# Optimization experiments

Measured on AMD Instinct MI355X. Metric: run time of the kernel, lower is better.

## Reference

```python
import jax, jax.numpy as jnp
import numpy as np


def setup_inputs() -> dict:
    key = jax.random.key(0)
    ks = jax.random.split(key, 8)
    B, L, E, D, A = 128, 196, 2048, 1024, 1024
    s_e = 1.0 / np.sqrt(E)
    s_d = 1.0 / np.sqrt(D)
    return {
        "encoder_outputs": jax.random.normal(ks[0], (B, L, E), jnp.float32),
        "decoder_hidden": jax.random.normal(ks[1], (B, D), jnp.float32),
        "Wq": jax.random.normal(ks[2], (A, E), jnp.float32) * s_e,
        "bq": jax.random.normal(ks[3], (A,), jnp.float32) * s_e,
        "Wv": jax.random.normal(ks[4], (A, E), jnp.float32) * s_e,
        "bv": jax.random.normal(ks[5], (A,), jnp.float32) * s_e,
        "Wd": jax.random.normal(ks[6], (A, D), jnp.float32) * s_d,
        "bd": jax.random.normal(ks[7], (A,), jnp.float32) * s_d,
    }


def reference(encoder_outputs, decoder_hidden, Wq, bq, Wv, bv, Wd, bd):
    # get_encoder_features: project encoder outputs to queries/values [B, L, A]
    enc_q = jnp.einsum('ble,ae->bla', encoder_outputs, Wq) + bq
    enc_v = jnp.einsum('ble,ae->bla', encoder_outputs, Wv) + bv
    # forward: project decoder hidden [B, A]
    dec_q = decoder_hidden @ Wd.T + bd
    # attn_energy = bmm(enc_q, dec_q) -> [B, L]; tanh then softmax over L
    energy = jnp.tanh(jnp.einsum('bla,ba->bl', enc_q, dec_q))
    weights = jax.nn.softmax(energy, axis=1)
    # context = bmm(weights, enc_v) -> [B, A]
    context = jnp.einsum('bl,bla->ba', weights, enc_v)
    return context
```

## Files before the change

### kernel.cpp

```cpp
#include <hip/hip_runtime.h>
#include <cstdint>
#include <cstddef>


template <bool BNC>
__global__ __launch_bounds__(256) void gemm_part(
    const float* __restrict__ A, const float* __restrict__ Bm,
    float* __restrict__ part, int M, int N, int K, int kPerZ) {
  __shared__ float As[32][132];
  __shared__ float Bs[32][68];
  const int t = threadIdx.x;
  const int tx = t & 7, ty = t >> 3;
  const int n0 = blockIdx.x * 64;
  const int m0 = blockIdx.y * 128;
  const int z  = blockIdx.z;
  const int k0 = z * kPerZ;

  float acc[4][8];
#pragma unroll
  for (int i = 0; i < 4; ++i)
#pragma unroll
    for (int j = 0; j < 8; ++j) acc[i][j] = 0.f;

  for (int kb = k0; kb < k0 + kPerZ; kb += 32) {
    __syncthreads();
    {
      int m = t >> 1, kq = (t & 1) * 16;
      const float* src = A + (size_t)(m0 + m) * K + (kb + kq);
      float4 v0 = *(const float4*)(src + 0);
      float4 v1 = *(const float4*)(src + 4);
      float4 v2 = *(const float4*)(src + 8);
      float4 v3 = *(const float4*)(src + 12);
      As[kq + 0][m] = v0.x; As[kq + 1][m] = v0.y; As[kq + 2][m] = v0.z; As[kq + 3][m] = v0.w;
      As[kq + 4][m] = v1.x; As[kq + 5][m] = v1.y; As[kq + 6][m] = v1.z; As[kq + 7][m] = v1.w;
      As[kq + 8][m] = v2.x; As[kq + 9][m] = v2.y; As[kq + 10][m] = v2.z; As[kq + 11][m] = v2.w;
      As[kq + 12][m] = v3.x; As[kq + 13][m] = v3.y; As[kq + 14][m] = v3.z; As[kq + 15][m] = v3.w;
    }
    if (BNC) {
      int kk = t >> 3, nq = (t & 7) * 8;
      const float* src = Bm + (size_t)(kb + kk) * N + (n0 + nq);
      float4 v0 = *(const float4*)(src + 0);
      float4 v1 = *(const float4*)(src + 4);
      *(float4*)&Bs[kk][nq + 0] = v0;
      *(float4*)&Bs[kk][nq + 4] = v1;
    } else {
      int n = t >> 2, kq = (t & 3) * 8;
      const float* src = Bm + (size_t)(n0 + n) * K + (kb + kq);
      float4 v0 = *(const float4*)(src + 0);
      float4 v1 = *(const float4*)(src + 4);
      Bs[kq + 0][n] = v0.x; Bs[kq + 1][n] = v0.y; Bs[kq + 2][n] = v0.z; Bs[kq + 3][n] = v0.w;
      Bs[kq + 4][n] = v1.x; Bs[kq + 5][n] = v1.y; Bs[kq + 6][n] = v1.z; Bs[kq + 7][n] = v1.w;
    }
    __syncthreads();
#pragma unroll 4
    for (int kk = 0; kk < 32; ++kk) {
      float av[4], bv[8];
      *(float4*)&av[0] = *(const float4*)&As[kk][ty * 4];
      *(float4*)&bv[0] = *(const float4*)&Bs[kk][tx * 8 + 0];
      *(float4*)&bv[4] = *(const float4*)&Bs[kk][tx * 8 + 4];
#pragma unroll
      for (int i = 0; i < 4; ++i)
#pragma unroll
        for (int j = 0; j < 8; ++j) acc[i][j] = fmaf(av[i], bv[j], acc[i][j]);
    }
  }
  float* dst = part + (size_t)z * M * N;
#pragma unroll
  for (int i = 0; i < 4; ++i) {
    int m = m0 + ty * 4 + i;
    float4 lo = make_float4(acc[i][0], acc[i][1], acc[i][2], acc[i][3]);
    float4 hi = make_float4(acc[i][4], acc[i][5], acc[i][6], acc[i][7]);
    *(float4*)&dst[(size_t)m * N + n0 + tx * 8 + 0] = lo;
    *(float4*)&dst[(size_t)m * N + n0 + tx * 8 + 4] = hi;
  }
}

__global__ __launch_bounds__(256) void reduce_part(
    const float* __restrict__ part, const float* __restrict__ bias,
    float* __restrict__ out, int MN, int N, int Z) {
  int i = blockIdx.x * 256 + threadIdx.x;
  if (i * 4 >= MN) return;
  float4 a = make_float4(0.f, 0.f, 0.f, 0.f);
  for (int z = 0; z < Z; ++z) {
    float4 v = *(const float4*)&part[(size_t)z * MN + i * 4];
    a.x += v.x; a.y += v.y; a.z += v.z; a.w += v.w;
  }
  if (bias) {
    int n = (i * 4) % N;
    float4 bb = *(const float4*)&bias[n];
    a.x += bb.x; a.y += bb.y; a.z += bb.z; a.w += bb.w;
  }
  *(float4*)&out[(size_t)i * 4] = a;
}

__global__ __launch_bounds__(256) void attn_pass(
    const float* __restrict__ x,
    const float* __restrict__ u,
    const float* __restrict__ dec_q,
    const float* __restrict__ bq,
    float* __restrict__ Yp,
    float* __restrict__ ss) {
  const int L = 196, E = 2048, A = 1024, RPB = 49;
  __shared__ float yS[4][2048];
  __shared__ float red[4];
  __shared__ float sred[4];
  const int t = threadIdx.x;
  const int lane = t & 63, w = t >> 6;
  const int b = blockIdx.x >> 2, q = blockIdx.x & 3;
  const int l0 = q * RPB;

  {
    const float* dq = dec_q + (size_t)b * A;
    float cp = 0.f;
#pragma unroll
    for (int j = 0; j < 4; ++j) cp = fmaf(bq[t + j * 256], dq[t + j * 256], cp);
    for (int off = 32; off; off >>= 1) cp += __shfl_xor(cp, off);
    if (lane == 0) red[w] = cp;
  }
  __syncthreads();
  const float cB = red[0] + red[1] + red[2] + red[3];

  float4 ur[8];
  const float* ub = u + (size_t)b * E;
#pragma unroll
  for (int i = 0; i < 8; ++i) ur[i] = *(const float4*)(ub + lane * 4 + i * 256);

  float4 y[8];
#pragma unroll
  for (int i = 0; i < 8; ++i) y[i] = make_float4(0.f, 0.f, 0.f, 0.f);
  float s = 0.f;

  for (int l = l0 + w; l < l0 + RPB; l += 4) {
    const float* xr = x + ((size_t)b * L + l) * E;
    float4 xv[8];
#pragma unroll
    for (int i = 0; i < 8; ++i) xv[i] = *(const float4*)(xr + lane * 4 + i * 256);
    float d = 0.f;
#pragma unroll
    for (int i = 0; i < 8; ++i) {
      d = fmaf(xv[i].x, ur[i].x, d);
      d = fmaf(xv[i].y, ur[i].y, d);
      d = fmaf(xv[i].z, ur[i].z, d);
      d = fmaf(xv[i].w, ur[i].w, d);
    }
    for (int off = 32; off; off >>= 1) d += __shfl_xor(d, off);
    float wj = __expf(tanhf(d + cB));
    s += wj;
#pragma unroll
    for (int i = 0; i < 8; ++i) {
      y[i].x = fmaf(wj, xv[i].x, y[i].x);
      y[i].y = fmaf(wj, xv[i].y, y[i].y);
      y[i].z = fmaf(wj, xv[i].z, y[i].z);
      y[i].w = fmaf(wj, xv[i].w, y[i].w);
    }
  }

#pragma unroll
  for (int i = 0; i < 8; ++i) *(float4*)&yS[w][lane * 4 + i * 256] = y[i];
  if (lane == 0) sred[w] = s;
  __syncthreads();

#pragma unroll
  for (int h = 0; h < 2; ++h) {
    int pos = t * 4 + h * 1024;
    float4 a0 = *(const float4*)&yS[0][pos];
    float4 a1 = *(const float4*)&yS[1][pos];
    float4 a2 = *(const float4*)&yS[2][pos];
    float4 a3 = *(const float4*)&yS[3][pos];
    float4 a = make_float4(a0.x + a1.x + a2.x + a3.x, a0.y + a1.y + a2.y + a3.y,
                           a0.z + a1.z + a2.z + a3.z, a0.w + a1.w + a2.w + a3.w);
    *(float4*)&Yp[(size_t)blockIdx.x * E + pos] = a;
  }
  if (t == 0) ss[blockIdx.x] = sred[0] + sred[1] + sred[2] + sred[3];
}

__global__ __launch_bounds__(256) void merge_y(
    const float* __restrict__ Yp, const float* __restrict__ ss,
    float* __restrict__ y) {
  const int E = 2048;
  int b = blockIdx.x, t = threadIdx.x;
  float S = ss[b * 4 + 0] + ss[b * 4 + 1] + ss[b * 4 + 2] + ss[b * 4 + 3];
  float inv = 1.f / S;
#pragma unroll
  for (int h = 0; h < 2; ++h) {
    int pos = t * 4 + h * 1024;
    float4 a = make_float4(0.f, 0.f, 0.f, 0.f);
#pragma unroll
    for (int qq = 0; qq < 4; ++qq) {
      float4 v = *(const float4*)&Yp[(size_t)(b * 4 + qq) * E + pos];
      a.x += v.x; a.y += v.y; a.z += v.z; a.w += v.w;
    }
    a.x *= inv; a.y *= inv; a.z *= inv; a.w *= inv;
    *(float4*)&y[(size_t)b * E + pos] = a;
  }
}

extern "C" void kernel_launch(void* const* d_in, const int* in_sizes, int n_in,
                              void* d_out, int out_size, void* d_ws, size_t ws_size,
                              hipStream_t stream) {
  const float* x  = (const float*)d_in[0];
  const float* dh = (const float*)d_in[1];
  const float* Wq = (const float*)d_in[2];
  const float* bq = (const float*)d_in[3];
  const float* Wv = (const float*)d_in[4];
  const float* bv = (const float*)d_in[5];
  const float* Wd = (const float*)d_in[6];
  const float* bd = (const float*)d_in[7];
  float* out = (float*)d_out;
  float* ws = (float*)d_ws;

  float* dec_q = ws;
  float* u     = ws + 131072;
  float* y     = ws + 393216;
  float* Yp    = ws + 655360;
  float* ssb   = ws + 1703936;
  float* part  = ws + 1705984;

  gemm_part<false><<<dim3(16, 1, 32), 256, 0, stream>>>(dh, Wd, part, 128, 1024, 1024, 32);
  reduce_part<<<dim3(128), 256, 0, stream>>>(part, bd, dec_q, 131072, 1024, 32);
  gemm_part<true><<<dim3(32, 1, 16), 256, 0, stream>>>(dec_q, Wq, part, 128, 2048, 1024, 64);
  reduce_part<<<dim3(256), 256, 0, stream>>>(part, nullptr, u, 262144, 2048, 16);
  attn_pass<<<dim3(512), 256, 0, stream>>>(x, u, dec_q, bq, Yp, ssb);
  merge_y<<<dim3(128), 256, 0, stream>>>(Yp, ssb, y);
  gemm_part<false><<<dim3(16, 1, 32), 256, 0, stream>>>(y, Wv, part, 128, 1024, 2048, 64);
  reduce_part<<<dim3(128), 256, 0, stream>>>(part, bv, out, 131072, 1024, 32);
}
```

Baseline: 368.8 us.

## Fuse all stages into one cooperative persistent kernel with grid syncs

Replaces the eight separate launches with a single cooperative kernel of 512 blocks that runs each stage and separates them with grid-wide syncs, falling back to the old multi-launch path if the cooperative launch fails. The attention stage now writes per-wave partial sums straight to global memory instead of reducing them through shared memory, and the merge stage sums 16 partials per batch row. This targets launch overhead and inter-kernel gaps between the small GEMM and reduce stages. In exchange it adds the cost of grid barriers, requires all 512 blocks to be co-resident, and increases the partial-sum traffic in the merge.

```diff
diff --git a/kernel.cpp b/kernel.cpp
--- a/kernel.cpp
+++ b/kernel.cpp
@@ -1,21 +1,20 @@
 #include <hip/hip_runtime.h>
+#include <hip/hip_cooperative_groups.h>
 #include <cstdint>
 #include <cstddef>
 
+namespace cg = cooperative_groups;
+
+
+struct SmGemm { float As[32][132]; float Bs[32][68]; };
 
 template <bool BNC>
-__global__ __launch_bounds__(256) void gemm_part(
+__device__ __forceinline__ void gemm_body(
     const float* __restrict__ A, const float* __restrict__ Bm,
-    float* __restrict__ part, int M, int N, int K, int kPerZ) {
-  __shared__ float As[32][132];
-  __shared__ float Bs[32][68];
-  const int t = threadIdx.x;
+    float* __restrict__ part, int N, int K, int kPerZ, int n0, int z,
+    SmGemm* sm, int t) {
   const int tx = t & 7, ty = t >> 3;
-  const int n0 = blockIdx.x * 64;
-  const int m0 = blockIdx.y * 128;
-  const int z  = blockIdx.z;
   const int k0 = z * kPerZ;
-
   float acc[4][8];
 #pragma unroll
   for (int i = 0; i < 4; ++i)
@@ -26,48 +25,48 @@
     __syncthreads();
     {
       int m = t >> 1, kq = (t & 1) * 16;
-      const float* src = A + (size_t)(m0 + m) * K + (kb + kq);
+      const float* src = A + (size_t)m * K + (kb + kq);
       float4 v0 = *(const float4*)(src + 0);
       float4 v1 = *(const float4*)(src + 4);
       float4 v2 = *(const float4*)(src + 8);
       float4 v3 = *(const float4*)(src + 12);
-      As[kq + 0][m] = v0.x; As[kq + 1][m] = v0.y; As[kq + 2][m] = v0.z; As[kq + 3][m] = v0.w;
-      As[kq + 4][m] = v1.x; As[kq + 5][m] = v1.y; As[kq + 6][m] = v1.z; As[kq + 7][m] = v1.w;
-      As[kq + 8][m] = v2.x; As[kq + 9][m] = v2.y; As[kq + 10][m] = v2.z; As[kq + 11][m] = v2.w;
-      As[kq + 12][m] = v3.x; As[kq + 13][m] = v3.y; As[kq + 14][m] = v3.z; As[kq + 15][m] = v3.w;
+      sm->As[kq + 0][m] = v0.x; sm->As[kq + 1][m] = v0.y; sm->As[kq + 2][m] = v0.z; sm->As[kq + 3][m] = v0.w;
+      sm->As[kq + 4][m] = v1.x; sm->As[kq + 5][m] = v1.y; sm->As[kq + 6][m] = v1.z; sm->As[kq + 7][m] = v1.w;
+      sm->As[kq + 8][m] = v2.x; sm->As[kq + 9][m] = v2.y; sm->As[kq + 10][m] = v2.z; sm->As[kq + 11][m] = v2.w;
+      sm->As[kq + 12][m] = v3.x; sm->As[kq + 13][m] = v3.y; sm->As[kq + 14][m] = v3.z; sm->As[kq + 15][m] = v3.w;
     }
     if (BNC) {
       int kk = t >> 3, nq = (t & 7) * 8;
       const float* src = Bm + (size_t)(kb + kk) * N + (n0 + nq);
       float4 v0 = *(const float4*)(src + 0);
       float4 v1 = *(const float4*)(src + 4);
-      *(float4*)&Bs[kk][nq + 0] = v0;
-      *(float4*)&Bs[kk][nq + 4] = v1;
+      *(float4*)&sm->Bs[kk][nq + 0] = v0;
+      *(float4*)&sm->Bs[kk][nq + 4] = v1;
     } else {
       int n = t >> 2, kq = (t & 3) * 8;
       const float* src = Bm + (size_t)(n0 + n) * K + (kb + kq);
       float4 v0 = *(const float4*)(src + 0);
       float4 v1 = *(const float4*)(src + 4);
-      Bs[kq + 0][n] = v0.x; Bs[kq + 1][n] = v0.y; Bs[kq + 2][n] = v0.z; Bs[kq + 3][n] = v0.w;
-      Bs[kq + 4][n] = v1.x; Bs[kq + 5][n] = v1.y; Bs[kq + 6][n] = v1.z; Bs[kq + 7][n] = v1.w;
+      sm->Bs[kq + 0][n] = v0.x; sm->Bs[kq + 1][n] = v0.y; sm->Bs[kq + 2][n] = v0.z; sm->Bs[kq + 3][n] = v0.w;
+      sm->Bs[kq + 4][n] = v1.x; sm->Bs[kq + 5][n] = v1.y; sm->Bs[kq + 6][n] = v1.z; sm->Bs[kq + 7][n] = v1.w;
     }
     __syncthreads();
 #pragma unroll 4
     for (int kk = 0; kk < 32; ++kk) {
       float av[4], bv[8];
-      *(float4*)&av[0] = *(const float4*)&As[kk][ty * 4];
-      *(float4*)&bv[0] = *(const float4*)&Bs[kk][tx * 8 + 0];
-      *(float4*)&bv[4] = *(const float4*)&Bs[kk][tx * 8 + 4];
+      *(float4*)&av[0] = *(const float4*)&sm->As[kk][ty * 4];
+      *(float4*)&bv[0] = *(const float4*)&sm->Bs[kk][tx * 8 + 0];
+      *(float4*)&bv[4] = *(const float4*)&sm->Bs[kk][tx * 8 + 4];
 #pragma unroll
       for (int i = 0; i < 4; ++i)
 #pragma unroll
         for (int j = 0; j < 8; ++j) acc[i][j] = fmaf(av[i], bv[j], acc[i][j]);
     }
   }
-  float* dst = part + (size_t)z * M * N;
+  float* dst = part + (size_t)z * 128 * N;
 #pragma unroll
   for (int i = 0; i < 4; ++i) {
-    int m = m0 + ty * 4 + i;
+    int m = ty * 4 + i;
     float4 lo = make_float4(acc[i][0], acc[i][1], acc[i][2], acc[i][3]);
     float4 hi = make_float4(acc[i][4], acc[i][5], acc[i][6], acc[i][7]);
     *(float4*)&dst[(size_t)m * N + n0 + tx * 8 + 0] = lo;
@@ -75,59 +74,47 @@
   }
 }
 
-__global__ __launch_bounds__(256) void reduce_part(
+__device__ __forceinline__ void reduce_body(
     const float* __restrict__ part, const float* __restrict__ bias,
-    float* __restrict__ out, int MN, int N, int Z) {
-  int i = blockIdx.x * 256 + threadIdx.x;
-  if (i * 4 >= MN) return;
-  float4 a = make_float4(0.f, 0.f, 0.f, 0.f);
-  for (int z = 0; z < Z; ++z) {
-    float4 v = *(const float4*)&part[(size_t)z * MN + i * 4];
-    a.x += v.x; a.y += v.y; a.z += v.z; a.w += v.w;
-  }
-  if (bias) {
-    int n = (i * 4) % N;
-    float4 bb = *(const float4*)&bias[n];
-    a.x += bb.x; a.y += bb.y; a.z += bb.z; a.w += bb.w;
-  }
-  *(float4*)&out[(size_t)i * 4] = a;
-}
-
-__global__ __launch_bounds__(256) void attn_pass(
-    const float* __restrict__ x,
-    const float* __restrict__ u,
-    const float* __restrict__ dec_q,
-    const float* __restrict__ bq,
-    float* __restrict__ Yp,
-    float* __restrict__ ss) {
+    float* __restrict__ outp, int MN, int N, int Z, int gtid) {
+  if (gtid * 4 < MN) {
+    float4 a = make_float4(0.f, 0.f, 0.f, 0.f);
+    for (int z = 0; z < Z; ++z) {
+      float4 v = *(const float4*)&part[(size_t)z * MN + gtid * 4];
+      a.x += v.x; a.y += v.y; a.z += v.z; a.w += v.w;
+    }
+    if (bias) {
+      int n = (gtid * 4) % N;
+      float4 bb = *(const float4*)&bias[n];
+      a.x += bb.x; a.y += bb.y; a.z += bb.z; a.w += bb.w;
+    }
+    *(float4*)&outp[(size_t)gtid * 4] = a;
+  }
+}
+
+__device__ __forceinline__ void attn_body(
+    const float* __restrict__ x, const float* __restrict__ u,
+    const float* __restrict__ dec_q, const float* __restrict__ bq,
+    float* __restrict__ Yp, float* __restrict__ ss, int bid, int t) {
   const int L = 196, E = 2048, A = 1024, RPB = 49;
-  __shared__ float yS[4][2048];
-  __shared__ float red[4];
-  __shared__ float sred[4];
-  const int t = threadIdx.x;
   const int lane = t & 63, w = t >> 6;
-  const int b = blockIdx.x >> 2, q = blockIdx.x & 3;
+  const int b = bid >> 2, q = bid & 3;
   const int l0 = q * RPB;
 
-  {
-    const float* dq = dec_q + (size_t)b * A;
-    float cp = 0.f;
-#pragma unroll
-    for (int j = 0; j < 4; ++j) cp = fmaf(bq[t + j * 256], dq[t + j * 256], cp);
-    for (int off = 32; off; off >>= 1) cp += __shfl_xor(cp, off);
-    if (lane == 0) red[w] = cp;
-  }
-  __syncthreads();
-  const float cB = red[0] + red[1] + red[2] + red[3];
+  const float* dq = dec_q + (size_t)b * A;
+  float cB = 0.f;
+#pragma unroll
+  for (int j = 0; j < 16; ++j) cB = fmaf(bq[lane + j * 64], dq[lane + j * 64], cB);
+  for (int off = 32; off; off >>= 1) cB += __shfl_xor(cB, off);
 
   float4 ur[8];
   const float* ub = u + (size_t)b * E;
 #pragma unroll
   for (int i = 0; i < 8; ++i) ur[i] = *(const float4*)(ub + lane * 4 + i * 256);
 
-  float4 y[8];
-#pragma unroll
-  for (int i = 0; i < 8; ++i) y[i] = make_float4(0.f, 0.f, 0.f, 0.f);
+  float4 ya[8];
+#pragma unroll
+  for (int i = 0; i < 8; ++i) ya[i] = make_float4(0.f, 0.f, 0.f, 0.f);
   float s = 0.f;
 
   for (int l = l0 + w; l < l0 + RPB; l += 4) {
@@ -148,51 +135,94 @@
     s += wj;
 #pragma unroll
     for (int i = 0; i < 8; ++i) {
-      y[i].x = fmaf(wj, xv[i].x, y[i].x);
-      y[i].y = fmaf(wj, xv[i].y, y[i].y);
-      y[i].z = fmaf(wj, xv[i].z, y[i].z);
-      y[i].w = fmaf(wj, xv[i].w, y[i].w);
-    }
-  }
-
-#pragma unroll
-  for (int i = 0; i < 8; ++i) *(float4*)&yS[w][lane * 4 + i * 256] = y[i];
-  if (lane == 0) sred[w] = s;
-  __syncthreads();
-
-#pragma unroll
-  for (int h = 0; h < 2; ++h) {
-    int pos = t * 4 + h * 1024;
-    float4 a0 = *(const float4*)&yS[0][pos];
-    float4 a1 = *(const float4*)&yS[1][pos];
-    float4 a2 = *(const float4*)&yS[2][pos];
-    float4 a3 = *(const float4*)&yS[3][pos];
-    float4 a = make_float4(a0.x + a1.x + a2.x + a3.x, a0.y + a1.y + a2.y + a3.y,
-                           a0.z + a1.z + a2.z + a3.z, a0.w + a1.w + a2.w + a3.w);
-    *(float4*)&Yp[(size_t)blockIdx.x * E + pos] = a;
-  }
-  if (t == 0) ss[blockIdx.x] = sred[0] + sred[1] + sred[2] + sred[3];
-}
-
-__global__ __launch_bounds__(256) void merge_y(
+      ya[i].x = fmaf(wj, xv[i].x, ya[i].x);
+      ya[i].y = fmaf(wj, xv[i].y, ya[i].y);
+      ya[i].z = fmaf(wj, xv[i].z, ya[i].z);
+      ya[i].w = fmaf(wj, xv[i].w, ya[i].w);
+    }
+  }
+#pragma unroll
+  for (int i = 0; i < 8; ++i)
+    *(float4*)&Yp[(size_t)(bid * 4 + w) * E + lane * 4 + i * 256] = ya[i];
+  if (lane == 0) ss[bid * 4 + w] = s;
+}
+
+__device__ __forceinline__ void merge_body(
     const float* __restrict__ Yp, const float* __restrict__ ss,
-    float* __restrict__ y) {
+    float* __restrict__ y, int b, int t) {
   const int E = 2048;
-  int b = blockIdx.x, t = threadIdx.x;
-  float S = ss[b * 4 + 0] + ss[b * 4 + 1] + ss[b * 4 + 2] + ss[b * 4 + 3];
+  float S = 0.f;
+#pragma unroll
+  for (int p = 0; p < 16; ++p) S += ss[b * 16 + p];
   float inv = 1.f / S;
 #pragma unroll
   for (int h = 0; h < 2; ++h) {
     int pos = t * 4 + h * 1024;
     float4 a = make_float4(0.f, 0.f, 0.f, 0.f);
 #pragma unroll
-    for (int qq = 0; qq < 4; ++qq) {
-      float4 v = *(const float4*)&Yp[(size_t)(b * 4 + qq) * E + pos];
+    for (int p = 0; p < 16; ++p) {
+      float4 v = *(const float4*)&Yp[(size_t)(b * 16 + p) * E + pos];
       a.x += v.x; a.y += v.y; a.z += v.z; a.w += v.w;
     }
     a.x *= inv; a.y *= inv; a.z *= inv; a.w *= inv;
     *(float4*)&y[(size_t)b * E + pos] = a;
   }
+}
+
+__global__ __launch_bounds__(256, 2) void fused_attn(
+    const float* __restrict__ x,  const float* __restrict__ dh,
+    const float* __restrict__ Wq, const float* __restrict__ bq,
+    const float* __restrict__ Wv, const float* __restrict__ bv,
+    const float* __restrict__ Wd, const float* __restrict__ bd,
+    float* __restrict__ out,
+    float* __restrict__ dec_q, float* __restrict__ u, float* __restrict__ y,
+    float* __restrict__ Yp, float* __restrict__ ss, float* __restrict__ part) {
+  cg::grid_group grid = cg::this_grid();
+  __shared__ SmGemm smg;
+  const int t = threadIdx.x;
+  const int bid = blockIdx.x;
+  const int gtid = bid * 256 + t;
+
+  gemm_body<false>(dh, Wd, part, 1024, 1024, 32, (bid & 15) * 64, bid >> 4, &smg, t);
+  grid.sync();
+  reduce_body(part, bd, dec_q, 131072, 1024, 32, gtid);
+  grid.sync();
+  gemm_body<true>(dec_q, Wq, part, 2048, 1024, 64, (bid & 31) * 64, bid >> 5, &smg, t);
+  grid.sync();
+  reduce_body(part, nullptr, u, 262144, 2048, 16, gtid);
+  grid.sync();
+  attn_body(x, u, dec_q, bq, Yp, ss, bid, t);
+  grid.sync();
+  if (bid < 128) merge_body(Yp, ss, y, bid, t);
+  grid.sync();
+  gemm_body<false>(y, Wv, part, 1024, 2048, 64, (bid & 15) * 64, bid >> 4, &smg, t);
+  grid.sync();
+  reduce_body(part, bv, out, 131072, 1024, 32, gtid);
+}
+
+template <bool BNC>
+__global__ __launch_bounds__(256) void k_gemm(
+    const float* __restrict__ A, const float* __restrict__ Bm,
+    float* __restrict__ part, int N, int K, int kPerZ) {
+  __shared__ SmGemm smg;
+  gemm_body<BNC>(A, Bm, part, N, K, kPerZ, blockIdx.x * 64, blockIdx.z, &smg,
+                 threadIdx.x);
+}
+__global__ __launch_bounds__(256) void k_reduce(
+    const float* __restrict__ part, const float* __restrict__ bias,
+    float* __restrict__ outp, int MN, int N, int Z) {
+  reduce_body(part, bias, outp, MN, N, Z, blockIdx.x * 256 + threadIdx.x);
+}
+__global__ __launch_bounds__(256) void k_attn(
+    const float* __restrict__ x, const float* __restrict__ u,
+    const float* __restrict__ dec_q, const float* __restrict__ bq,
+    float* __restrict__ Yp, float* __restrict__ ss) {
+  attn_body(x, u, dec_q, bq, Yp, ss, blockIdx.x, threadIdx.x);
+}
+__global__ __launch_bounds__(256) void k_merge(
+    const float* __restrict__ Yp, const float* __restrict__ ss,
+    float* __restrict__ y) {
+  merge_body(Yp, ss, y, blockIdx.x, threadIdx.x);
 }
 
 extern "C" void kernel_launch(void* const* d_in, const int* in_sizes, int n_in,
@@ -212,16 +242,24 @@
   float* dec_q = ws;
   float* u     = ws + 131072;
   float* y     = ws + 393216;
-  float* Yp    = ws + 655360;
-  float* ssb   = ws + 1703936;
-  float* part  = ws + 1705984;
-
-  gemm_part<false><<<dim3(16, 1, 32), 256, 0, stream>>>(dh, Wd, part, 128, 1024, 1024, 32);
-  reduce_part<<<dim3(128), 256, 0, stream>>>(part, bd, dec_q, 131072, 1024, 32);
-  gemm_part<true><<<dim3(32, 1, 16), 256, 0, stream>>>(dec_q, Wq, part, 128, 2048, 1024, 64);
-  reduce_part<<<dim3(256), 256, 0, stream>>>(part, nullptr, u, 262144, 2048, 16);
-  attn_pass<<<dim3(512), 256, 0, stream>>>(x, u, dec_q, bq, Yp, ssb);
-  merge_y<<<dim3(128), 256, 0, stream>>>(Yp, ssb, y);
-  gemm_part<false><<<dim3(16, 1, 32), 256, 0, stream>>>(y, Wv, part, 128, 1024, 2048, 64);
-  reduce_part<<<dim3(128), 256, 0, stream>>>(part, bv, out, 131072, 1024, 32);
-}
+  float* ssb   = ws + 655360;
+  float* part  = ws + 657408;
+  float* Yp    = part;
+
+  void* args[] = {
+      (void*)&x,  (void*)&dh, (void*)&Wq, (void*)&bq, (void*)&Wv, (void*)&bv,
+      (void*)&Wd, (void*)&bd, (void*)&out,
+      (void*)&dec_q, (void*)&u, (void*)&y, (void*)&Yp, (void*)&ssb, (void*)&part};
+  hipError_t err = hipLaunchCooperativeKernel((void*)fused_attn, dim3(512),
+                                              dim3(256), args, 0, stream);
+  if (err != hipSuccess) {
+    k_gemm<false><<<dim3(16, 1, 32), 256, 0, stream>>>(dh, Wd, part, 1024, 1024, 32);
+    k_reduce<<<dim3(128), 256, 0, stream>>>(part, bd, dec_q, 131072, 1024, 32);
+    k_gemm<true><<<dim3(32, 1, 16), 256, 0, stream>>>(dec_q, Wq, part, 2048, 1024, 64);
+    k_reduce<<<dim3(256), 256, 0, stream>>>(part, nullptr, u, 262144, 2048, 16);
+    k_attn<<<dim3(512), 256, 0, stream>>>(x, u, dec_q, bq, Yp, ssb);
+    k_merge<<<dim3(128), 256, 0, stream>>>(Yp, ssb, y);
+    k_gemm<false><<<dim3(16, 1, 32), 256, 0, stream>>>(y, Wv, part, 1024, 2048, 64);
+    k_reduce<<<dim3(128), 256, 0, stream>>>(part, bv, out, 131072, 1024, 32);
+  }
+}
```

Measured after the change: 805.2 us. 2.18x slower.
